# Optimization experiments

Measured on AMD Instinct MI355X. Metric: run time of the kernel, lower is better.

Reference implementation:

```python
import jax, jax.numpy as jnp
import numpy as np

NUM_STEPS = 96  # ray samples M; ProSTGrid's step count, fixed for static shapes


def _transform_mat3x4(pose):
    # pose: [B,6] -> rigid transform [B,3,4], matches set_matrix (Rz@Ry@Rx@T)
    B = pose.shape[0]
    rx, ry, rz, tx, ty, tz = [pose[:, i] for i in range(6)]
    o = jnp.zeros((B,), pose.dtype)
    l = jnp.ones((B,), pose.dtype)
    cx, sx = jnp.cos(rx), jnp.sin(rx)
    cy, sy = jnp.cos(ry), jnp.sin(ry)
    cz, sz = jnp.cos(rz), jnp.sin(rz)
    Rx = jnp.stack([jnp.stack([l, o, o, o], -1), jnp.stack([o, cx, -sx, o], -1),
                    jnp.stack([o, sx, cx, o], -1), jnp.stack([o, o, o, l], -1)], 1)
    Ry = jnp.stack([jnp.stack([cy, o, sy, o], -1), jnp.stack([o, l, o, o], -1),
                    jnp.stack([-sy, o, cy, o], -1), jnp.stack([o, o, o, l], -1)], 1)
    Rz = jnp.stack([jnp.stack([cz, -sz, o, o], -1), jnp.stack([sz, cz, o, o], -1),
                    jnp.stack([o, o, l, o], -1), jnp.stack([o, o, o, l], -1)], 1)
    T = jnp.stack([jnp.stack([l, o, o, tx], -1), jnp.stack([o, l, o, ty], -1),
                   jnp.stack([o, o, l, tz], -1), jnp.stack([o, o, o, l], -1)], 1)
    M = Rz @ Ry @ Rx @ T
    return M[:, :3, :]


def _raydist_range(T, corner_pt, src):
    # inv_pose_vec + raydist_range
    t = T[:, :3, 3]
    R = T[:, :3, :3]
    pt = corner_pt - t[:, None, :]
    inv_pt = pt @ jnp.linalg.inv(R)          # pt.bmm(inv(R))
    inv_pt = inv_pt.at[:, :, 2].set(src - inv_pt[:, :, 2])
    dist = jnp.sqrt(jnp.sum(inv_pt * inv_pt, axis=-1))
    return jnp.min(dist), jnp.max(dist)


def _make_grid(H, W, M, dmin, dmax, src, det, pix_spacing):
    # Cone-beam sampling grid: source at (0,0,src), detector plane z = src-det.
    ys = (jnp.arange(H, dtype=jnp.float32) - (H - 1) / 2.0) * pix_spacing
    xs = (jnp.arange(W, dtype=jnp.float32) - (W - 1) / 2.0) * pix_spacing
    yy, xx = jnp.meshgrid(ys, xs, indexing='ij')          # [H,W]
    dz = jnp.full_like(xx, -det)
    dirv = jnp.stack([xx, yy, dz], -1)                    # detector - source
    dirv = dirv / jnp.linalg.norm(dirv, axis=-1, keepdims=True)
    dists = jnp.linspace(dmin, dmax, M)                   # [M]
    src_pt = jnp.stack([jnp.zeros(()), jnp.zeros(()), src])
    pts = src_pt + dirv[:, :, None, :] * dists[None, None, :, None]  # [H,W,M,3]
    ones = jnp.ones(pts.shape[:-1] + (1,), pts.dtype)
    return jnp.concatenate([pts, ones], -1).reshape(1, H * W * M, 4)


def _trilinear_5d(vol, grid):
    # faithful port of _bilinear_interpolate_no_torch_5D (8-corner gather+blend)
    B, C, D, Hv, Wv = vol.shape
    im_flat = jnp.transpose(vol, (0, 2, 3, 4, 1)).reshape(-1, C)  # [B*D*H*W, C]
    _, oD, oH, oW, _ = grid.shape
    x = (Wv * (grid[..., 0] * 0.5 + 0.5)).reshape(-1)
    y = (Hv * (grid[..., 1] * 0.5 + 0.5)).reshape(-1)
    z = (D * (grid[..., 2] * 0.5 + 0.5)).reshape(-1)
    oob = ~((x >= 0) & (x <= Wv) & (y >= 0) & (y <= Hv) & (z >= 0) & (z <= D))
    x0 = jnp.clip(jnp.floor(x), 0, Wv - 1); x1 = jnp.clip(jnp.floor(x) + 1, 0, Wv - 1)
    y0 = jnp.clip(jnp.floor(y), 0, Hv - 1); y1 = jnp.clip(jnp.floor(y) + 1, 0, Hv - 1)
    z0 = jnp.clip(jnp.floor(z), 0, D - 1);  z1 = jnp.clip(jnp.floor(z) + 1, 0, D - 1)
    base = jnp.repeat(jnp.arange(B, dtype=jnp.int32) * (D * Hv * Wv), oD * oH * oW)
    def gather(zc, yc, xc):
        idx = base + zc.astype(jnp.int32) * (Hv * Wv) + yc.astype(jnp.int32) * Wv + xc.astype(jnp.int32)
        return im_flat[idx]
    Ia, Ib = gather(z0, y0, x0), gather(z0, y0, x1)
    Ic, Id = gather(z0, y1, x0), gather(z0, y1, x1)
    Ie, If = gather(z1, y0, x0), gather(z1, y0, x1)
    Ig, Ih = gather(z1, y1, x0), gather(z1, y1, x1)
    wa = ((x1 - x) * (y1 - y) * (z1 - z))[:, None]
    wb = ((x - x0) * (y1 - y) * (z1 - z))[:, None]
    wc = ((x1 - x) * (y - y0) * (z1 - z))[:, None]
    wd = ((x - x0) * (y - y0) * (z1 - z))[:, None]
    we = ((x1 - x) * (y1 - y) * (z - z0))[:, None]
    wf = ((x - x0) * (y1 - y) * (z - z0))[:, None]
    wg = ((x1 - x) * (y - y0) * (z - z0))[:, None]
    wh = ((x - x0) * (y - y0) * (z - z0))[:, None]
    acc = wa * Ia + wb * Ib + wc * Ic + wd * Id + we * Ie + wf * If + wg * Ig + wh * Ih
    acc = jnp.where(oob[:, None], 0.0, acc)
    out = acc.reshape(B, oD, oH, oW, C)
    return jnp.transpose(out, (0, 4, 1, 2, 3))


def setup_inputs() -> dict:
    key = jax.random.key(0)
    k1, k2, k3 = jax.random.split(key, 3)
    D, H, W = 128, 256, 256
    ct = jax.random.normal(k1, (1, 1, D, D, D), jnp.float32)
    fixed = jax.random.normal(k2, (1, 1, H, W), jnp.float32)
    pose = jax.random.normal(k3, (1, 6), jnp.float32) * 0.1
    corner_pt = jnp.array([[[sx, sy, sz] for sx in (-1.0, 1.0) for sy in (-1.0, 1.0)
                            for sz in (-1.0, 1.0)]], jnp.float32)  # [1,8,3]
    # param = (src, det, pix_spacing, step_size), volume normalized to [-1,1]^3
    param = jnp.array([4.0, 8.0, 4.0 / W, 0.02], jnp.float32)
    return {"ct": ct, "fixed": fixed, "pose": pose, "corner_pt": corner_pt,
            "param": param, "H": H, "W": W}


def reference(ct, fixed, pose, corner_pt, param, H, W):
    src, det, pix_spacing = param[0], param[1], param[2]
    T = _transform_mat3x4(pose)                                # [1,3,4]
    dmin, dmax = _raydist_range(T, corner_pt, src)
    dmin = jax.lax.stop_gradient(dmin)                         # .data in torch
    dmax = jax.lax.stop_gradient(dmax)
    grid = _make_grid(H, W, NUM_STEPS, dmin, dmax, src, det, pix_spacing)  # [1,HWM,4]
    grid_trans = (grid @ jnp.swapaxes(T, 1, 2)).reshape(1, H, W, NUM_STEPS, 3)
    x_3d = _trilinear_5d(ct, grid_trans)                       # [1,C,H,W,M]
    moving = jnp.sum(x_3d, axis=-1)                            # integrate along rays
    return moving
```

## Files before the change

kernel.cpp:

```cpp
#include <hip/hip_runtime.h>
#include <hip/hip_fp16.h>

#define NUM_STEPS 96
#define SPLIT 4
#define SPT (NUM_STEPS / SPLIT)
#define VD 128
#define VSLICE (VD * VD)
#define NVOX (VD * VD * VD)
#define VOL8_BYTES ((size_t)NVOX * 16)

__global__ __launch_bounds__(256) void prost_pack8_kernel(
    const float* __restrict__ ct, uint4* __restrict__ vol8)
{
    const int i = blockIdx.x * 256 + threadIdx.x;
    const int x = i & (VD - 1);
    const int y = (i >> 7) & (VD - 1);
    const int z = i >> 14;
    const int xp = min(x + 1, VD - 1);
    const int yp = min(y + 1, VD - 1);
    const int zp = min(z + 1, VD - 1);

    const float* r00 = ct + (z  << 14) + (y  << 7);
    const float* r01 = ct + (z  << 14) + (yp << 7);
    const float* r10 = ct + (zp << 14) + (y  << 7);
    const float* r11 = ct + (zp << 14) + (yp << 7);

    const __half2 ab = __floats2half2_rn(r00[x], r00[xp]);
    const __half2 cd = __floats2half2_rn(r01[x], r01[xp]);
    const __half2 ef = __floats2half2_rn(r10[x], r10[xp]);
    const __half2 gh = __floats2half2_rn(r11[x], r11[xp]);

    uint4 q;
    q.x = *reinterpret_cast<const unsigned int*>(&ab);
    q.y = *reinterpret_cast<const unsigned int*>(&cd);
    q.z = *reinterpret_cast<const unsigned int*>(&ef);
    q.w = *reinterpret_cast<const unsigned int*>(&gh);
    vol8[i] = q;
}

__device__ __forceinline__ void prost_setup(
    const float* __restrict__ pose, const float* __restrict__ corner,
    const float* __restrict__ param, int h, int w, int H, int W,
    float& Ax, float& Bx, float& Ay, float& By, float& Az, float& Bz,
    float& dmin, float& step)
{
    const float rx = pose[0], ry = pose[1], rz = pose[2];
    const float tx = pose[3], ty = pose[4], tz = pose[5];
    const float cx = cosf(rx), sx = sinf(rx);
    const float cy = cosf(ry), sy = sinf(ry);
    const float cz = cosf(rz), sz = sinf(rz);

    const float r00 = cz * cy;
    const float r01 = -sz * cx + cz * sy * sx;
    const float r02 = sz * sx + cz * sy * cx;
    const float r10 = sz * cy;
    const float r11 = cz * cx + sz * sy * sx;
    const float r12 = -cz * sx + sz * sy * cx;
    const float r20 = -sy;
    const float r21 = cy * sx;
    const float r22 = cy * cx;

    const float t0 = r00 * tx + r01 * ty + r02 * tz;
    const float t1 = r10 * tx + r11 * ty + r12 * tz;
    const float t2 = r20 * tx + r21 * ty + r22 * tz;

    const float src = param[0];
    const float det = param[1];
    const float pix = param[2];

    float dmax = -1e30f;
    dmin = 1e30f;
    #pragma unroll
    for (int c = 0; c < 8; ++c) {
        const float px = corner[c * 3 + 0] - t0;
        const float py = corner[c * 3 + 1] - t1;
        const float pz = corner[c * 3 + 2] - t2;
        const float ix = r00 * px + r01 * py + r02 * pz;
        const float iy = r10 * px + r11 * py + r12 * pz;
        float iz = r20 * px + r21 * py + r22 * pz;
        iz = src - iz;
        const float d = sqrtf(ix * ix + iy * iy + iz * iz);
        dmin = fminf(dmin, d);
        dmax = fmaxf(dmax, d);
    }

    const float ys = ((float)h - (float)(H - 1) * 0.5f) * pix;
    const float xs = ((float)w - (float)(W - 1) * 0.5f) * pix;
    const float dz = -det;
    const float invn = 1.0f / sqrtf(xs * xs + ys * ys + dz * dz);
    const float nx = xs * invn;
    const float ny = ys * invn;
    const float nz = dz * invn;

    Ax = 64.0f * (r00 * nx + r01 * ny + r02 * nz);
    Bx = 64.0f * (r02 * src + t0) + 64.0f;
    Ay = 64.0f * (r10 * nx + r11 * ny + r12 * nz);
    By = 64.0f * (r12 * src + t1) + 64.0f;
    Az = 64.0f * (r20 * nx + r21 * ny + r22 * nz);
    Bz = 64.0f * (r22 * src + t2) + 64.0f;

    step = (dmax - dmin) / (float)(NUM_STEPS - 1);
}

__global__ __launch_bounds__(256) void prost_fwd_h8_kernel(
    const uint4* __restrict__ vol8,
    const float* __restrict__ pose,
    const float* __restrict__ corner,
    const float* __restrict__ param,
    const int* __restrict__ Hp,
    const int* __restrict__ Wp,
    float* __restrict__ out,
    int n)
{
    const int gid = blockIdx.x * blockDim.x + threadIdx.x;
    const int idx = gid >> 2;
    const int seg = gid & 3;
    if (idx >= n) return;

    const int H = *Hp;
    const int W = *Wp;
    const int h = idx / W;
    const int w = idx % W;

    float Ax, Bx, Ay, By, Az, Bz, dmin, step;
    prost_setup(pose, corner, param, h, w, H, W, Ax, Bx, Ay, By, Az, Bz, dmin, step);

    const int m0 = seg * SPT;
    float acc = 0.0f;

    #pragma unroll 8
    for (int k = 0; k < SPT; ++k) {
        const float d = dmin + step * (float)(m0 + k);
        const float X = Ax * d + Bx;
        const float Y = Ay * d + By;
        const float Z = Az * d + Bz;

        const bool inb = (X >= 0.0f) & (X <= 128.0f) &
                         (Y >= 0.0f) & (Y <= 128.0f) &
                         (Z >= 0.0f) & (Z <= 128.0f);

        const float fx = floorf(X), fy = floorf(Y), fz = floorf(Z);
        const float x0 = fminf(fmaxf(fx,        0.0f), 127.0f);
        const float x1 = fminf(fmaxf(fx + 1.0f, 0.0f), 127.0f);
        const float y0 = fminf(fmaxf(fy,        0.0f), 127.0f);
        const float y1 = fminf(fmaxf(fy + 1.0f, 0.0f), 127.0f);
        const float z0 = fminf(fmaxf(fz,        0.0f), 127.0f);
        const float z1 = fminf(fmaxf(fz + 1.0f, 0.0f), 127.0f);

        const float wx1 = X - x0, wx0 = x1 - X;
        const float wy1 = Y - y0, wy0 = y1 - Y;
        const float wz0 = inb ? (z1 - Z) : 0.0f;
        const float wz1 = inb ? (Z - z0) : 0.0f;

        const int cell = ((int)z0 << 14) + ((int)y0 << 7) + (int)x0;
        const uint4 q = vol8[cell];

        const __half2 ab = *reinterpret_cast<const __half2*>(&q.x);
        const __half2 cd = *reinterpret_cast<const __half2*>(&q.y);
        const __half2 ef = *reinterpret_cast<const __half2*>(&q.z);
        const __half2 gh = *reinterpret_cast<const __half2*>(&q.w);

        const float Ia = __low2float(ab), Ib = __high2float(ab);
        const float Ic = __low2float(cd), Id = __high2float(cd);
        const float Ie = __low2float(ef), If = __high2float(ef);
        const float Ig = __low2float(gh), Ih = __high2float(gh);

        acc += wz0 * (wy0 * (wx0 * Ia + wx1 * Ib) +
                      wy1 * (wx0 * Ic + wx1 * Id)) +
               wz1 * (wy0 * (wx0 * Ie + wx1 * If) +
                      wy1 * (wx0 * Ig + wx1 * Ih));
    }

    acc += __shfl_xor(acc, 1);
    acc += __shfl_xor(acc, 2);

    if (seg == 0) out[idx] = acc;
}

__global__ __launch_bounds__(256) void prost_fwd_kernel(
    const float* __restrict__ ct,
    const float* __restrict__ pose,
    const float* __restrict__ corner,
    const float* __restrict__ param,
    const int* __restrict__ Hp,
    const int* __restrict__ Wp,
    float* __restrict__ out,
    int n)
{
    const int gid = blockIdx.x * blockDim.x + threadIdx.x;
    const int idx = gid >> 2;
    const int seg = gid & 3;
    if (idx >= n) return;

    const int H = *Hp;
    const int W = *Wp;
    const int h = idx / W;
    const int w = idx % W;

    float Ax, Bx, Ay, By, Az, Bz, dmin, step;
    prost_setup(pose, corner, param, h, w, H, W, Ax, Bx, Ay, By, Az, Bz, dmin, step);

    const int m0 = seg * SPT;
    float acc = 0.0f;

    #pragma unroll 4
    for (int k = 0; k < SPT; ++k) {
        const float d = dmin + step * (float)(m0 + k);
        const float X = Ax * d + Bx;
        const float Y = Ay * d + By;
        const float Z = Az * d + Bz;

        const bool inb = (X >= 0.0f) & (X <= 128.0f) &
                         (Y >= 0.0f) & (Y <= 128.0f) &
                         (Z >= 0.0f) & (Z <= 128.0f);

        const float fx = floorf(X), fy = floorf(Y), fz = floorf(Z);
        const float x0 = fminf(fmaxf(fx,        0.0f), 127.0f);
        const float x1 = fminf(fmaxf(fx + 1.0f, 0.0f), 127.0f);
        const float y0 = fminf(fmaxf(fy,        0.0f), 127.0f);
        const float y1 = fminf(fmaxf(fy + 1.0f, 0.0f), 127.0f);
        const float z0 = fminf(fmaxf(fz,        0.0f), 127.0f);
        const float z1 = fminf(fmaxf(fz + 1.0f, 0.0f), 127.0f);

        const float wx1 = X - x0, wx0 = x1 - X;
        const float wy1 = Y - y0, wy0 = y1 - Y;
        const float wz0 = z1 - Z, wz1 = Z - z0;

        const int ix0 = (int)x0, ix1 = (int)x1;
        const int iy0 = (int)y0, iy1 = (int)y1;
        const int iz0 = (int)z0, iz1 = (int)z1;

        const float* p00 = ct + (iz0 << 14) + (iy0 << 7);
        const float* p01 = ct + (iz0 << 14) + (iy1 << 7);
        const float* p10 = ct + (iz1 << 14) + (iy0 << 7);
        const float* p11 = ct + (iz1 << 14) + (iy1 << 7);

        const float Ia = p00[ix0], Ib = p00[ix1];
        const float Ic = p01[ix0], Id = p01[ix1];
        const float Ie = p10[ix0], If = p10[ix1];
        const float Ig = p11[ix0], Ih = p11[ix1];

        const float s =
            wz0 * (wy0 * (wx0 * Ia + wx1 * Ib) + wy1 * (wx0 * Ic + wx1 * Id)) +
            wz1 * (wy0 * (wx0 * Ie + wx1 * If) + wy1 * (wx0 * Ig + wx1 * Ih));
        acc += inb ? s : 0.0f;
    }

    acc += __shfl_xor(acc, 1);
    acc += __shfl_xor(acc, 2);

    if (seg == 0) out[idx] = acc;
}

extern "C" void kernel_launch(void* const* d_in, const int* in_sizes, int n_in,
                              void* d_out, int out_size, void* d_ws, size_t ws_size,
                              hipStream_t stream) {
    const float* ct     = (const float*)d_in[0];
    const float* pose   = (const float*)d_in[2];
    const float* corner = (const float*)d_in[3];
    const float* param  = (const float*)d_in[4];
    const int*   Hp     = (const int*)d_in[5];
    const int*   Wp     = (const int*)d_in[6];
    float* out = (float*)d_out;

    const int n = out_size;
    const int total = n * SPLIT;
    const int block = 256;
    const int grid = (total + block - 1) / block;

    if (ws_size >= VOL8_BYTES) {
        uint4* vol8 = (uint4*)d_ws;
        prost_pack8_kernel<<<NVOX / 256, 256, 0, stream>>>(ct, vol8);
        prost_fwd_h8_kernel<<<grid, block, 0, stream>>>(vol8, pose, corner, param,
                                                        Hp, Wp, out, n);
    } else {
        prost_fwd_kernel<<<grid, block, 0, stream>>>(ct, pose, corner, param,
                                                     Hp, Wp, out, n);
    }
}
```

Before: 38.56 us.

## Pack volume as 8-byte fp16 x-z pairs and split rays eight ways

The packed volume layout shrinks from 16 bytes per voxel (a full 2x2x2 corner set) to 8 bytes per voxel holding the x/x+1 pair for slices z and z+1. Each sample now does two 8-byte loads (rows y0 and y1) instead of one 16-byte load. This halves the pack-kernel write traffic and the workspace footprint, which should improve cache hit rates. The ray-march kernel splits each ray across 8 threads instead of 4, fully unrolls the shorter loop, remaps block IDs in an XCD-aware way, and sets launch bounds for occupancy; the trade-off is more gather instructions per sample.

```diff
diff --git a/kernel.cpp b/kernel.cpp
--- a/kernel.cpp
+++ b/kernel.cpp
@@ -2,40 +2,45 @@
 #include <hip/hip_fp16.h>
 
 #define NUM_STEPS 96
-#define SPLIT 4
+#define SPLIT 8
 #define SPT (NUM_STEPS / SPLIT)
 #define VD 128
-#define VSLICE (VD * VD)
 #define NVOX (VD * VD * VD)
-#define VOL8_BYTES ((size_t)NVOX * 16)
-
-__global__ __launch_bounds__(256) void prost_pack8_kernel(
-    const float* __restrict__ ct, uint4* __restrict__ vol8)
-{
-    const int i = blockIdx.x * 256 + threadIdx.x;
-    const int x = i & (VD - 1);
-    const int y = (i >> 7) & (VD - 1);
-    const int z = i >> 14;
-    const int xp = min(x + 1, VD - 1);
-    const int yp = min(y + 1, VD - 1);
+#define VOLH_BYTES ((size_t)NVOX * 8)
+
+__global__ __launch_bounds__(256) void prost_packh_kernel(
+    const float* __restrict__ ct, uint2* __restrict__ vol)
+{
+    const int g  = blockIdx.x * 256 + threadIdx.x;
+    const int xq = g & 31;
+    const int y  = (g >> 5) & 127;
+    const int z  = g >> 12;
+    const int x  = xq << 2;
     const int zp = min(z + 1, VD - 1);
 
-    const float* r00 = ct + (z  << 14) + (y  << 7);
-    const float* r01 = ct + (z  << 14) + (yp << 7);
-    const float* r10 = ct + (zp << 14) + (y  << 7);
-    const float* r11 = ct + (zp << 14) + (yp << 7);
-
-    const __half2 ab = __floats2half2_rn(r00[x], r00[xp]);
-    const __half2 cd = __floats2half2_rn(r01[x], r01[xp]);
-    const __half2 ef = __floats2half2_rn(r10[x], r10[xp]);
-    const __half2 gh = __floats2half2_rn(r11[x], r11[xp]);
-
-    uint4 q;
-    q.x = *reinterpret_cast<const unsigned int*>(&ab);
-    q.y = *reinterpret_cast<const unsigned int*>(&cd);
-    q.z = *reinterpret_cast<const unsigned int*>(&ef);
-    q.w = *reinterpret_cast<const unsigned int*>(&gh);
-    vol8[i] = q;
+    const float* r0 = ct + (z  << 14) + (y << 7);
+    const float* r1 = ct + (zp << 14) + (y << 7);
+
+    const float4 f0 = *reinterpret_cast<const float4*>(r0 + x);
+    const float4 f1 = *reinterpret_cast<const float4*>(r1 + x);
+    const float  e0 = r0[min(x + 4, VD - 1)];
+    const float  e1 = r1[min(x + 4, VD - 1)];
+
+    const float a0[5] = {f0.x, f0.y, f0.z, f0.w, e0};
+    const float a1[5] = {f1.x, f1.y, f1.z, f1.w, e1};
+
+    unsigned int c[8];
+    #pragma unroll
+    for (int j = 0; j < 4; ++j) {
+        const __half2 lo = __floats2half2_rn(a0[j], a0[j + 1]);
+        const __half2 hi = __floats2half2_rn(a1[j], a1[j + 1]);
+        c[2 * j]     = *reinterpret_cast<const unsigned int*>(&lo);
+        c[2 * j + 1] = *reinterpret_cast<const unsigned int*>(&hi);
+    }
+
+    uint4* dst = reinterpret_cast<uint4*>(vol + (size_t)g * 4);
+    dst[0] = make_uint4(c[0], c[1], c[2], c[3]);
+    dst[1] = make_uint4(c[4], c[5], c[6], c[7]);
 }
 
 __device__ __forceinline__ void prost_setup(
@@ -102,8 +107,8 @@
     step = (dmax - dmin) / (float)(NUM_STEPS - 1);
 }
 
-__global__ __launch_bounds__(256) void prost_fwd_h8_kernel(
-    const uint4* __restrict__ vol8,
+__global__ __launch_bounds__(256, 8) void prost_fwd_h4_kernel(
+    const uint2* __restrict__ vol,
     const float* __restrict__ pose,
     const float* __restrict__ corner,
     const float* __restrict__ param,
@@ -112,9 +117,16 @@
     float* __restrict__ out,
     int n)
 {
-    const int gid = blockIdx.x * blockDim.x + threadIdx.x;
-    const int idx = gid >> 2;
-    const int seg = gid & 3;
+    const int nblk = gridDim.x;
+    int bid = blockIdx.x;
+    if ((nblk & 7) == 0) {
+        const int c = nblk >> 3;
+        bid = (bid & 7) * c + (bid >> 3);
+    }
+
+    const int tid = threadIdx.x;
+    const int idx = bid * 32 + (tid >> 3);
+    const int seg = tid & 7;
     if (idx >= n) return;
 
     const int H = *Hp;
@@ -128,7 +140,7 @@
     const int m0 = seg * SPT;
     float acc = 0.0f;
 
-    #pragma unroll 8
+    #pragma unroll
     for (int k = 0; k < SPT; ++k) {
         const float d = dmin + step * (float)(m0 + k);
         const float X = Ax * d + Bx;
@@ -152,17 +164,18 @@
         const float wz0 = inb ? (z1 - Z) : 0.0f;
         const float wz1 = inb ? (Z - z0) : 0.0f;
 
-        const int cell = ((int)z0 << 14) + ((int)y0 << 7) + (int)x0;
-        const uint4 q = vol8[cell];
-
-        const __half2 ab = *reinterpret_cast<const __half2*>(&q.x);
-        const __half2 cd = *reinterpret_cast<const __half2*>(&q.y);
-        const __half2 ef = *reinterpret_cast<const __half2*>(&q.z);
-        const __half2 gh = *reinterpret_cast<const __half2*>(&q.w);
+        const int base = ((int)z0 << 14) + (int)x0;
+        const uint2 qa = vol[base + ((int)y0 << 7)];
+        const uint2 qb = vol[base + ((int)y1 << 7)];
+
+        const __half2 ab = *reinterpret_cast<const __half2*>(&qa.x);
+        const __half2 ef = *reinterpret_cast<const __half2*>(&qa.y);
+        const __half2 cd = *reinterpret_cast<const __half2*>(&qb.x);
+        const __half2 gh = *reinterpret_cast<const __half2*>(&qb.y);
 
         const float Ia = __low2float(ab), Ib = __high2float(ab);
+        const float Ie = __low2float(ef), If = __high2float(ef);
         const float Ic = __low2float(cd), Id = __high2float(cd);
-        const float Ie = __low2float(ef), If = __high2float(ef);
         const float Ig = __low2float(gh), Ih = __high2float(gh);
 
         acc += wz0 * (wy0 * (wx0 * Ia + wx1 * Ib) +
@@ -173,6 +186,7 @@
 
     acc += __shfl_xor(acc, 1);
     acc += __shfl_xor(acc, 2);
+    acc += __shfl_xor(acc, 4);
 
     if (seg == 0) out[idx] = acc;
 }
@@ -200,11 +214,11 @@
     float Ax, Bx, Ay, By, Az, Bz, dmin, step;
     prost_setup(pose, corner, param, h, w, H, W, Ax, Bx, Ay, By, Az, Bz, dmin, step);
 
-    const int m0 = seg * SPT;
+    const int m0 = seg * (NUM_STEPS / 4);
     float acc = 0.0f;
 
     #pragma unroll 4
-    for (int k = 0; k < SPT; ++k) {
+    for (int k = 0; k < NUM_STEPS / 4; ++k) {
         const float d = dmin + step * (float)(m0 + k);
         const float X = Ax * d + Bx;
         const float Y = Ay * d + By;
@@ -264,17 +278,16 @@
     float* out = (float*)d_out;
 
     const int n = out_size;
-    const int total = n * SPLIT;
-    const int block = 256;
-    const int grid = (total + block - 1) / block;
-
-    if (ws_size >= VOL8_BYTES) {
-        uint4* vol8 = (uint4*)d_ws;
-        prost_pack8_kernel<<<NVOX / 256, 256, 0, stream>>>(ct, vol8);
-        prost_fwd_h8_kernel<<<grid, block, 0, stream>>>(vol8, pose, corner, param,
+
+    if (ws_size >= VOLH_BYTES) {
+        uint2* vol = (uint2*)d_ws;
+        prost_packh_kernel<<<(NVOX / 4) / 256, 256, 0, stream>>>(ct, vol);
+        const int blocks = (n * SPLIT + 255) / 256;
+        prost_fwd_h4_kernel<<<blocks, 256, 0, stream>>>(vol, pose, corner, param,
                                                         Hp, Wp, out, n);
     } else {
-        prost_fwd_kernel<<<grid, block, 0, stream>>>(ct, pose, corner, param,
-                                                     Hp, Wp, out, n);
-    }
-}
+        const int total = n * 4;
+        prost_fwd_kernel<<<(total + 255) / 256, 256, 0, stream>>>(ct, pose, corner,
+                                                                  param, Hp, Wp, out, n);
+    }
+}
```

Measured after the change: 47.53 us. 1.23x slower.
